# Kernel optimization log

Measured on AMD Instinct MI355X. Metric: run time of the kernel, lower is better.

## Reference

```python
import math
import jax, jax.numpy as jnp
import numpy as np

N = 512
C_S, C_Z, C_H, H, PQ, PV = 384, 128, 16, 12, 4, 8
INF, EPS = 1e5, 1e-8


def _quat_to_rot(q):
    # q: [N,4] unnormalized quaternions -> [N,3,3] rotation matrices
    q = q / jnp.linalg.norm(q, axis=-1, keepdims=True)
    w, x, y, z = q[:, 0], q[:, 1], q[:, 2], q[:, 3]
    return jnp.stack([
        jnp.stack([1 - 2 * (y * y + z * z), 2 * (x * y - w * z), 2 * (x * z + w * y)], -1),
        jnp.stack([2 * (x * y + w * z), 1 - 2 * (x * x + z * z), 2 * (y * z - w * x)], -1),
        jnp.stack([2 * (x * z - w * y), 2 * (y * z + w * x), 1 - 2 * (x * x + y * y)], -1),
    ], -2)


def setup_inputs() -> dict:
    key = jax.random.key(0)
    ks = jax.random.split(key, 16)
    sc = 0.02
    inp = {
        "s": jax.random.normal(ks[0], (N, C_S), jnp.float32),
        "z": jax.random.normal(ks[1], (N, N, C_Z), jnp.float32),
        "rot": _quat_to_rot(jax.random.normal(ks[2], (N, 4), jnp.float32)),
        "trans": jax.random.normal(ks[3], (N, 3), jnp.float32) * 10.0,
        "mask": jnp.ones((N,), jnp.float32),
        "Wq": jax.random.normal(ks[4], (C_S, H * C_H), jnp.float32) * sc,
        "bq": jnp.zeros((H * C_H,), jnp.float32),
        "Wkv": jax.random.normal(ks[5], (C_S, 2 * H * C_H), jnp.float32) * sc,
        "bkv": jnp.zeros((2 * H * C_H,), jnp.float32),
        "Wqp": jax.random.normal(ks[6], (C_S, H * 3 * PQ), jnp.float32) * sc,
        "bqp": jnp.zeros((H * 3 * PQ,), jnp.float32),
        "Wkvp": jax.random.normal(ks[7], (C_S, H * 3 * (PQ + PV)), jnp.float32) * sc,
        "bkvp": jnp.zeros((H * 3 * (PQ + PV),), jnp.float32),
        "Wb": jax.random.normal(ks[8], (C_Z, H), jnp.float32) * sc,
        "bb": jnp.zeros((H,), jnp.float32),
        "head_weights": jnp.full((H,), math.log(math.e - 1.0), jnp.float32),
        "Wout": jax.random.normal(ks[9], (H * (C_Z + C_H + PV * 4), C_S), jnp.float32) * sc,
        "bout": jnp.zeros((C_S,), jnp.float32),
    }
    return inp


def _ipa(s, z, rot, trans, mask, Wq, bq, Wkv, bkv, Wqp, bqp, Wkvp, bkvp, Wb, bb, head_weights, Wout, bout):
    q = (s @ Wq + bq).reshape(N, H, C_H)
    kv = (s @ Wkv + bkv).reshape(N, H, 2 * C_H)
    k, v = kv[..., :C_H], kv[..., C_H:]

    def proj_pts(W, b, P):
        # torch: split last dim into 3 chunks, stack on -1 -> layout [N, 3, H, P] -> [N, H, P, 3]
        pl = (s @ W + b).reshape(N, 3, H, P).transpose(0, 2, 3, 1)
        return jnp.einsum('nij,nhpj->nhpi', rot, pl) + trans[:, None, None, :]

    q_pts = proj_pts(Wqp, bqp, PQ)                    # [N,H,PQ,3]
    kv_pts = proj_pts(Wkvp, bkvp, PQ + PV)            # [N,H,PQ+PV,3]
    k_pts, v_pts = kv_pts[..., :PQ, :], kv_pts[..., PQ:, :]

    b_bias = z @ Wb + bb                              # [N,N,H]
    a = jnp.einsum('ihc,jhc->hij', q, k) * math.sqrt(1.0 / (3 * C_H))
    a = a + math.sqrt(1.0 / 3) * b_bias.transpose(2, 0, 1)

    d2 = jnp.sum((q_pts[:, None] - k_pts[None]) ** 2, axis=-1)   # [i,j,H,PQ]
    hw = jax.nn.softplus(head_weights) * math.sqrt(1.0 / (3 * (PQ * 9.0 / 2)))
    pt_att = -0.5 * jnp.sum(d2 * hw[None, None, :, None], axis=-1)  # [i,j,H]

    sq_mask = INF * (mask[:, None] * mask[None, :] - 1.0)
    a = jax.nn.softmax(a + pt_att.transpose(2, 0, 1) + sq_mask[None], axis=-1)  # [H,i,j]

    o = jnp.einsum('hij,jhc->ihc', a, v).reshape(N, H * C_H)
    o_pt = jnp.einsum('hij,jhpc->ihpc', a, v_pts)                 # [i,H,PV,3]
    o_pt = jnp.einsum('nji,nhpj->nhpi', rot, o_pt - trans[:, None, None, :])  # invert_apply
    o_pt_norm = jnp.sqrt(jnp.sum(o_pt ** 2, axis=-1) + EPS).reshape(N, H * PV)
    o_pt_flat = o_pt.reshape(N, H * PV, 3)
    o_pair = jnp.einsum('hij,ijc->ihc', a, z).reshape(N, H * C_Z)

    cat = jnp.concatenate(
        [o, o_pt_flat[..., 0], o_pt_flat[..., 1], o_pt_flat[..., 2], o_pt_norm, o_pair], axis=-1)
    return cat @ Wout + bout


def reference(s, z, rot, trans, mask, Wq, bq, Wkv, bkv, Wqp, bqp, Wkvp, bkvp, Wb, bb, head_weights, Wout, bout):
    return _ipa(s, z, rot, trans, mask, Wq, bq, Wkv, bkv, Wqp, bqp, Wkvp, bkvp, Wb, bb, head_weights, Wout, bout)
```

## Files before the change

### kernel.cpp

```cpp
#include <hip/hip_runtime.h>
#include <math.h>

#define NN 512
#define CS 384
#define CZ 128
#define CH 16
#define HH 12
#define PQ 4
#define PV 8

typedef float f32x4 __attribute__((ext_vector_type(4)));
typedef __bf16 bf16x8 __attribute__((ext_vector_type(8)));

__global__ void k_repack(const float* __restrict__ Wq,  const float* __restrict__ bq,
                         const float* __restrict__ Wkv, const float* __restrict__ bkv,
                         const float* __restrict__ Wqp, const float* __restrict__ bqp,
                         const float* __restrict__ Wkvp,const float* __restrict__ bkvp,
                         float* __restrict__ Wcat, float* __restrict__ bcat)
{
    const int total = CS * 1152;
    for (int idx = blockIdx.x * blockDim.x + threadIdx.x; idx < total; idx += gridDim.x * blockDim.x) {
        int kk = idx / 1152, n = idx % 1152;
        float vv;
        if (n < 192)      vv = Wq  [kk * 192 + n];
        else if (n < 576) vv = Wkv [kk * 384 + (n - 192)];
        else if (n < 720) vv = Wqp [kk * 144 + (n - 576)];
        else              vv = Wkvp[kk * 432 + (n - 720)];
        Wcat[idx] = vv;
    }
    int n = blockIdx.x * blockDim.x + threadIdx.x;
    if (n < 1152) {
        float vv;
        if (n < 192)      vv = bq  [n];
        else if (n < 576) vv = bkv [n - 192];
        else if (n < 720) vv = bqp [n - 576];
        else              vv = bkvp[n - 720];
        bcat[n] = vv;
    }
}

__global__ void k_proj(const float* __restrict__ s, const float* __restrict__ Wcat,
                       const float* __restrict__ bcat,
                       float* __restrict__ q, float* __restrict__ k_t, float* __restrict__ v,
                       float* __restrict__ qp_raw, float* __restrict__ kvp_raw)
{
    __shared__ float As[64 * 68];
    __shared__ float Bs[64 * 64];

    int tx = threadIdx.x & 15;
    int ty = threadIdx.x >> 4;
    int n0 = blockIdx.x * 64;
    int m0 = blockIdx.y * 64;

    float acc[4][4];
    #pragma unroll
    for (int r = 0; r < 4; ++r)
        #pragma unroll
        for (int cc = 0; cc < 4; ++cc) acc[r][cc] = 0.f;

    for (int kb = 0; kb < CS; kb += 64) {
        #pragma unroll
        for (int e = 0; e < 16; ++e) {
            int idx = e * 256 + threadIdx.x;
            int m = idx >> 6, kk = idx & 63;
            As[m * 68 + kk] = s[(size_t)(m0 + m) * CS + kb + kk];
        }
        #pragma unroll
        for (int e = 0; e < 16; ++e) {
            int idx = e * 256 + threadIdx.x;
            int kk = idx >> 6, n = idx & 63;
            Bs[kk * 64 + n] = Wcat[(size_t)(kb + kk) * 1152 + n0 + n];
        }
        __syncthreads();

        for (int kk = 0; kk < 64; kk += 4) {
            f32x4 a[4], b[4];
            #pragma unroll
            for (int r = 0; r < 4; ++r)
                a[r] = *(const f32x4*)&As[(ty * 4 + r) * 68 + kk];
            #pragma unroll
            for (int kq = 0; kq < 4; ++kq)
                b[kq] = *(const f32x4*)&Bs[(kk + kq) * 64 + tx * 4];
            #pragma unroll
            for (int kq = 0; kq < 4; ++kq)
                #pragma unroll
                for (int r = 0; r < 4; ++r)
                    #pragma unroll
                    for (int cc = 0; cc < 4; ++cc)
                        acc[r][cc] += a[r][kq] * b[kq][cc];
        }
        __syncthreads();
    }

    #pragma unroll
    for (int r = 0; r < 4; ++r) {
        int i = m0 + ty * 4 + r;
        #pragma unroll
        for (int cc = 0; cc < 4; ++cc) {
            int col = n0 + tx * 4 + cc;
            float val = acc[r][cc] + bcat[col];
            if (col < 192) {
                q[i * 192 + col] = val;
            } else if (col < 576) {
                int lc = col - 192;
                int h = lc / 32, w = lc % 32;
                if (w < CH) k_t[(h * CH + w) * NN + i] = val;
                else        v[(i * HH + h) * CH + (w - CH)] = val;
            } else if (col < 720) {
                qp_raw[i * 144 + (col - 576)] = val;
            } else {
                kvp_raw[i * 432 + (col - 720)] = val;
            }
        }
    }
}

__global__ void k_pts_transform(const float* __restrict__ qp_raw, const float* __restrict__ kvp_raw,
                                const float* __restrict__ rot, const float* __restrict__ trans,
                                float* __restrict__ q_pts, float* __restrict__ k_pts_t,
                                float* __restrict__ v_pts)
{
    int idx = blockIdx.x * blockDim.x + threadIdx.x;
    const int total = NN * HH * 16;
    if (idx >= total) return;
    int i = idx / (HH * 16);
    int r = idx % (HH * 16);
    int h = r / 16;
    int p = r % 16;

    float R[9], t3[3];
    for (int a = 0; a < 9; ++a) R[a] = rot[i * 9 + a];
    for (int a = 0; a < 3; ++a) t3[a] = trans[i * 3 + a];

    float x, y, zc;
    if (p < PQ) {
        x  = qp_raw[i * 144 + 0 * 48 + h * PQ + p];
        y  = qp_raw[i * 144 + 1 * 48 + h * PQ + p];
        zc = qp_raw[i * 144 + 2 * 48 + h * PQ + p];
    } else {
        int pp = p - PQ;
        x  = kvp_raw[i * 432 + 0 * 144 + h * 12 + pp];
        y  = kvp_raw[i * 432 + 1 * 144 + h * 12 + pp];
        zc = kvp_raw[i * 432 + 2 * 144 + h * 12 + pp];
    }
    float ox = R[0] * x + R[1] * y + R[2] * zc + t3[0];
    float oy = R[3] * x + R[4] * y + R[5] * zc + t3[1];
    float oz = R[6] * x + R[7] * y + R[8] * zc + t3[2];

    if (p < PQ) {
        int o = ((i * HH + h) * PQ + p) * 3;
        q_pts[o] = ox; q_pts[o + 1] = oy; q_pts[o + 2] = oz;
    } else {
        int pp = p - PQ;
        if (pp < PQ) {
            int rb = (h * PQ + pp) * 3;
            k_pts_t[(size_t)(rb + 0) * NN + i] = ox;
            k_pts_t[(size_t)(rb + 1) * NN + i] = oy;
            k_pts_t[(size_t)(rb + 2) * NN + i] = oz;
        } else {
            int o = ((i * HH + h) * PV + (pp - PQ)) * 3;
            v_pts[o] = ox; v_pts[o + 1] = oy; v_pts[o + 2] = oz;
        }
    }
}

__global__ void k_bias(const float* __restrict__ z, const float* __restrict__ Wb,
                       float* __restrict__ b_bias)
{
    int i = blockIdx.x;
    int lane = threadIdx.x & 63;
    int wave = threadIdx.x >> 6;
    int col  = lane & 15;
    int quad = lane >> 4;

    bf16x8 bfrag[4];
    #pragma unroll
    for (int kc = 0; kc < 4; ++kc) {
        #pragma unroll
        for (int jj = 0; jj < 8; ++jj) {
            int c = kc * 32 + quad * 8 + jj;
            float wv = (col < HH) ? Wb[c * HH + col] : 0.0f;
            bfrag[kc][jj] = (__bf16)wv;
        }
    }

    for (int tt = 0; tt < 8; ++tt) {
        int j0 = (wave + 4 * tt) * 16;
        const float* zrow = z + ((size_t)i * NN + j0 + col) * CZ;
        f32x4 acc = {0.f, 0.f, 0.f, 0.f};
        #pragma unroll
        for (int kc = 0; kc < 4; ++kc) {
            float4 z0 = *(const float4*)(zrow + kc * 32 + quad * 8);
            float4 z1 = *(const float4*)(zrow + kc * 32 + quad * 8 + 4);
            bf16x8 afrag;
            afrag[0] = (__bf16)z0.x; afrag[1] = (__bf16)z0.y;
            afrag[2] = (__bf16)z0.z; afrag[3] = (__bf16)z0.w;
            afrag[4] = (__bf16)z1.x; afrag[5] = (__bf16)z1.y;
            afrag[6] = (__bf16)z1.z; afrag[7] = (__bf16)z1.w;
            acc = __builtin_amdgcn_mfma_f32_16x16x32_bf16(afrag, bfrag[kc], acc, 0, 0, 0);
        }
        if (col < HH) {
            #pragma unroll
            for (int r = 0; r < 4; ++r) {
                int j = j0 + quad * 4 + r;
                b_bias[((size_t)col * NN + i) * NN + j] = acc[r];
            }
        }
    }
}

__global__ void k_logits(const float* __restrict__ b_bias, const float* __restrict__ bb,
                         const float* __restrict__ q, const float* __restrict__ k_t,
                         const float* __restrict__ q_pts, const float* __restrict__ k_pts_t,
                         const float* __restrict__ head_weights,
                         const float* __restrict__ mask,
                         float* __restrict__ a_out)
{
    __shared__ float lgs[HH][NN];
    __shared__ float q_lds[HH * CH];
    __shared__ float qp_lds[HH * PQ * 3];
    __shared__ float hw_lds[HH];

    int i = blockIdx.x;
    int j = threadIdx.x;

    for (int t = j; t < HH * CH; t += 512) q_lds[t] = q[i * HH * CH + t];
    for (int t = j; t < HH * PQ * 3; t += 512) qp_lds[t] = q_pts[i * HH * PQ * 3 + t];
    if (j < HH) {
        float x = head_weights[j];
        hw_lds[j] = log1pf(expf(x)) * sqrtf(1.0f / 54.0f);
    }
    __syncthreads();

    const float qk_scale = sqrtf(1.0f / 48.0f);
    const float b_scale  = sqrtf(1.0f / 3.0f);
    float sqm = 100000.0f * (mask[i] * mask[j] - 1.0f);

    #pragma unroll
    for (int h = 0; h < HH; ++h) {
        float bias_h = b_bias[((size_t)h * NN + i) * NN + j] + bb[h];
        float acc = 0.f;
        #pragma unroll
        for (int c = 0; c < CH; ++c)
            acc += q_lds[h * CH + c] * k_t[(size_t)(h * CH + c) * NN + j];
        float s2 = 0.f;
        #pragma unroll
        for (int p = 0; p < PQ; ++p) {
            int rb = (h * PQ + p) * 3;
            float dx = qp_lds[rb + 0] - k_pts_t[(size_t)(rb + 0) * NN + j];
            float dy = qp_lds[rb + 1] - k_pts_t[(size_t)(rb + 1) * NN + j];
            float dz = qp_lds[rb + 2] - k_pts_t[(size_t)(rb + 2) * NN + j];
            s2 += dx * dx + dy * dy + dz * dz;
        }
        lgs[h][j] = acc * qk_scale + b_scale * bias_h - 0.5f * hw_lds[h] * s2 + sqm;
    }
    __syncthreads();

    int wave = j >> 6, lane = j & 63;
    for (int row = wave; row < HH; row += 8) {
        float vals[8];
        float m = -1e30f;
        #pragma unroll
        for (int u = 0; u < 8; ++u) { vals[u] = lgs[row][lane + u * 64]; m = fmaxf(m, vals[u]); }
        #pragma unroll
        for (int off = 32; off >= 1; off >>= 1) m = fmaxf(m, __shfl_xor(m, off));
        float ssum = 0.f;
        #pragma unroll
        for (int u = 0; u < 8; ++u) { vals[u] = expf(vals[u] - m); ssum += vals[u]; }
        #pragma unroll
        for (int off = 32; off >= 1; off >>= 1) ssum += __shfl_xor(ssum, off);
        float inv = 1.0f / ssum;
        #pragma unroll
        for (int u = 0; u < 8; ++u) lgs[row][lane + u * 64] = vals[u] * inv;
    }
    __syncthreads();

    #pragma unroll
    for (int h = 0; h < HH; ++h)
        a_out[((size_t)h * NN + i) * NN + j] = lgs[h][j];
}

__global__ void k_out_ov(const float* __restrict__ a, const float* __restrict__ v,
                         const float* __restrict__ v_pts,
                         const float* __restrict__ rot, const float* __restrict__ trans,
                         float* __restrict__ cat)
{
    __shared__ float a_lds[HH][NN];
    __shared__ float opt_lds[HH * PV * 3];
    int i = blockIdx.x;
    for (int h = 0; h < HH; ++h)
        for (int j = threadIdx.x; j < NN; j += 256)
            a_lds[h][j] = a[((size_t)h * NN + i) * NN + j];
    __syncthreads();

    for (int out = threadIdx.x; out < 480; out += 256) {
        float acc = 0.f;
        if (out < 192) {
            int h = out / CH;
            for (int j = 0; j < NN; ++j)
                acc += a_lds[h][j] * v[(size_t)j * 192 + out];
            cat[(size_t)i * 2112 + out] = acc;
        } else {
            int r = out - 192;
            int h = r / (PV * 3);
            for (int j = 0; j < NN; ++j)
                acc += a_lds[h][j] * v_pts[(size_t)j * (HH * PV * 3) + r];
            opt_lds[r] = acc;
        }
    }
    __syncthreads();

    if (threadIdx.x < HH * PV) {
        int hp = threadIdx.x;
        float R[9], t3[3];
        for (int a2 = 0; a2 < 9; ++a2) R[a2] = rot[i * 9 + a2];
        for (int a2 = 0; a2 < 3; ++a2) t3[a2] = trans[i * 3 + a2];
        float gx = opt_lds[hp * 3 + 0] - t3[0];
        float gy = opt_lds[hp * 3 + 1] - t3[1];
        float gz = opt_lds[hp * 3 + 2] - t3[2];
        float lx = R[0] * gx + R[3] * gy + R[6] * gz;
        float ly = R[1] * gx + R[4] * gy + R[7] * gz;
        float lz = R[2] * gx + R[5] * gy + R[8] * gz;
        float* crow = cat + (size_t)i * 2112;
        crow[192 + 0 * 96 + hp] = lx;
        crow[192 + 1 * 96 + hp] = ly;
        crow[192 + 2 * 96 + hp] = lz;
        crow[480 + hp] = sqrtf(lx * lx + ly * ly + lz * lz + 1e-8f);
    }
}

#define ALDS_STRIDE 516
__global__ void __launch_bounds__(256)
k_out_pair(const float* __restrict__ a, const float* __restrict__ z,
           float* __restrict__ cat)
{
    __shared__ float a_lds[HH * ALDS_STRIDE];

    int i = blockIdx.x;
    int tid = threadIdx.x;
    int lane = tid & 63;
    int wave = tid >> 6;
    int col  = lane & 15;
    int quad = lane >> 4;

    for (int t = tid; t < HH * NN; t += 256) {
        int h = t >> 9, j = t & 511;
        a_lds[h * ALDS_STRIDE + j] = a[((size_t)h * NN + i) * NN + j];
    }
    __syncthreads();

    int hc = (col < HH) ? col : (HH - 1);
    f32x4 acc0 = {0.f, 0.f, 0.f, 0.f};
    f32x4 acc1 = {0.f, 0.f, 0.f, 0.f};
    int c0 = (wave * 2 + 0) * 16 + col;
    int c1 = (wave * 2 + 1) * 16 + col;

    for (int ks = 0; ks < 16; ++ks) {
        int k0 = ks * 32 + quad * 8;
        const float* arow = &a_lds[hc * ALDS_STRIDE + k0];
        bf16x8 af;
        #pragma unroll
        for (int jj = 0; jj < 8; ++jj) af[jj] = (__bf16)arow[jj];

        const float* zrow = z + ((size_t)i * NN + k0) * CZ;
        bf16x8 bf0, bf1;
        #pragma unroll
        for (int jj = 0; jj < 8; ++jj) bf0[jj] = (__bf16)zrow[(size_t)jj * CZ + c0];
        #pragma unroll
        for (int jj = 0; jj < 8; ++jj) bf1[jj] = (__bf16)zrow[(size_t)jj * CZ + c1];

        acc0 = __builtin_amdgcn_mfma_f32_16x16x32_bf16(af, bf0, acc0, 0, 0, 0);
        acc1 = __builtin_amdgcn_mfma_f32_16x16x32_bf16(af, bf1, acc1, 0, 0, 0);
    }

    float* crow = cat + (size_t)i * 2112 + 576;
    #pragma unroll
    for (int r = 0; r < 4; ++r) {
        int h = quad * 4 + r;
        if (h < HH) {
            crow[h * CZ + c0] = acc0[r];
            crow[h * CZ + c1] = acc1[r];
        }
    }
}

__global__ void k_final(const float* __restrict__ cat, const float* __restrict__ Wout,
                        const float* __restrict__ bout, float* __restrict__ out)
{
    __shared__ float As[64 * 52];
    __shared__ float Bs[48 * 64];

    int tx = threadIdx.x & 15;
    int ty = threadIdx.x >> 4;
    int n0 = blockIdx.x * 64;
    int m0 = blockIdx.y * 64;
    int k0 = blockIdx.z * 528;

    float acc[4][4];
    #pragma unroll
    for (int r = 0; r < 4; ++r)
        #pragma unroll
        for (int cc = 0; cc < 4; ++cc) acc[r][cc] = 0.f;

    for (int stage = 0; stage < 11; ++stage) {
        int kb = k0 + stage * 48;
        #pragma unroll
        for (int e = 0; e < 12; ++e) {
            int idx = e * 256 + threadIdx.x;
            int m = idx / 48, kk = idx % 48;
            As[m * 52 + kk] = cat[(size_t)(m0 + m) * 2112 + kb + kk];
        }
        #pragma unroll
        for (int e = 0; e < 12; ++e) {
            int idx = e * 256 + threadIdx.x;
            int kk = idx >> 6, n = idx & 63;
            Bs[kk * 64 + n] = Wout[(size_t)(kb + kk) * 384 + n0 + n];
        }
        __syncthreads();

        for (int kk = 0; kk < 48; kk += 4) {
            f32x4 a[4], b[4];
            #pragma unroll
            for (int r = 0; r < 4; ++r)
                a[r] = *(const f32x4*)&As[(ty * 4 + r) * 52 + kk];
            #pragma unroll
            for (int kq = 0; kq < 4; ++kq)
                b[kq] = *(const f32x4*)&Bs[(kk + kq) * 64 + tx * 4];
            #pragma unroll
            for (int kq = 0; kq < 4; ++kq)
                #pragma unroll
                for (int r = 0; r < 4; ++r)
                    #pragma unroll
                    for (int cc = 0; cc < 4; ++cc)
                        acc[r][cc] += a[r][kq] * b[kq][cc];
        }
        __syncthreads();
    }

    bool add_bias = (blockIdx.z == 0);
    #pragma unroll
    for (int r = 0; r < 4; ++r) {
        int m = m0 + ty * 4 + r;
        #pragma unroll
        for (int cc = 0; cc < 4; ++cc) {
            int n = n0 + tx * 4 + cc;
            float val = acc[r][cc] + (add_bias ? bout[n] : 0.f);
            atomicAdd(&out[(size_t)m * 384 + n], val);
        }
    }
}

extern "C" void kernel_launch(void* const* d_in, const int* in_sizes, int n_in,
                              void* d_out, int out_size, void* d_ws, size_t ws_size,
                              hipStream_t stream)
{
    const float* s     = (const float*)d_in[0];
    const float* z     = (const float*)d_in[1];
    const float* rot   = (const float*)d_in[2];
    const float* trans = (const float*)d_in[3];
    const float* mask  = (const float*)d_in[4];
    const float* Wq    = (const float*)d_in[5];
    const float* bq    = (const float*)d_in[6];
    const float* Wkv   = (const float*)d_in[7];
    const float* bkv   = (const float*)d_in[8];
    const float* Wqp   = (const float*)d_in[9];
    const float* bqp   = (const float*)d_in[10];
    const float* Wkvp  = (const float*)d_in[11];
    const float* bkvp  = (const float*)d_in[12];
    const float* Wb    = (const float*)d_in[13];
    const float* bb    = (const float*)d_in[14];
    const float* hw    = (const float*)d_in[15];
    const float* Wout  = (const float*)d_in[16];
    const float* bout  = (const float*)d_in[17];
    float* out = (float*)d_out;

    float* ws = (float*)d_ws;
    float* q       = ws;
    float* k_t     = ws + 98304;
    float* v       = ws + 196608;
    float* qp_raw  = ws + 294912;
    float* kvp_raw = ws + 368640;
    float* q_pts   = ws + 589824;
    float* k_pts_t = ws + 663552;
    float* v_pts   = ws + 737280;
    float* a_buf   = ws + 884736;
    float* b_bias  = ws + 4030464;
    float* cat     = ws + 7176192;
    float* Wcat    = ws + 8257536;
    float* bcat    = ws + 8699904;

    hipMemsetAsync(out, 0, (size_t)NN * CS * sizeof(float), stream);

    hipLaunchKernelGGL(k_repack, dim3(512), dim3(256), 0, stream,
                       Wq, bq, Wkv, bkv, Wqp, bqp, Wkvp, bkvp, Wcat, bcat);
    hipLaunchKernelGGL(k_proj, dim3(18, 8), dim3(256), 0, stream,
                       s, Wcat, bcat, q, k_t, v, qp_raw, kvp_raw);
    hipLaunchKernelGGL(k_pts_transform, dim3(384), dim3(256), 0, stream,
                       qp_raw, kvp_raw, rot, trans, q_pts, k_pts_t, v_pts);
    hipLaunchKernelGGL(k_bias, dim3(NN), dim3(256), 0, stream, z, Wb, b_bias);
    hipLaunchKernelGGL(k_logits, dim3(NN), dim3(512), 0, stream,
                       b_bias, bb, q, k_t, q_pts, k_pts_t, hw, mask, a_buf);
    hipLaunchKernelGGL(k_out_ov, dim3(NN), dim3(256), 0, stream,
                       a_buf, v, v_pts, rot, trans, cat);
    hipLaunchKernelGGL(k_out_pair, dim3(NN), dim3(256), 0, stream, a_buf, z, cat);
    hipLaunchKernelGGL(k_final, dim3(6, 8, 4), dim3(256), 0, stream, cat, Wout, bout, out);
}
```

Before: 413.4 us.

## Fuse pair bias, logits, softmax and output aggregation into one attention kernel

Result: slower. 431.9 us (+4.5%).

```diff
diff --git a/kernel.cpp b/kernel.cpp
--- a/kernel.cpp
+++ b/kernel.cpp
@@ -8,9 +8,11 @@
 #define HH 12
 #define PQ 4
 #define PV 8
+#define LGS_S 516
 
 typedef float f32x4 __attribute__((ext_vector_type(4)));
 typedef __bf16 bf16x8 __attribute__((ext_vector_type(8)));
+typedef __bf16 bf16x4 __attribute__((ext_vector_type(4)));
 
 __global__ void k_repack(const float* __restrict__ Wq,  const float* __restrict__ bq,
                          const float* __restrict__ Wkv, const float* __restrict__ bkv,
@@ -164,85 +166,19 @@
     }
 }
 
-__global__ void k_bias(const float* __restrict__ z, const float* __restrict__ Wb,
-                       float* __restrict__ b_bias)
-{
-    int i = blockIdx.x;
-    int lane = threadIdx.x & 63;
-    int wave = threadIdx.x >> 6;
-    int col  = lane & 15;
-    int quad = lane >> 4;
-
-    bf16x8 bfrag[4];
-    #pragma unroll
-    for (int kc = 0; kc < 4; ++kc) {
-        #pragma unroll
-        for (int jj = 0; jj < 8; ++jj) {
-            int c = kc * 32 + quad * 8 + jj;
-            float wv = (col < HH) ? Wb[c * HH + col] : 0.0f;
-            bfrag[kc][jj] = (__bf16)wv;
-        }
-    }
-
-    for (int tt = 0; tt < 8; ++tt) {
-        int j0 = (wave + 4 * tt) * 16;
-        const float* zrow = z + ((size_t)i * NN + j0 + col) * CZ;
-        f32x4 acc = {0.f, 0.f, 0.f, 0.f};
-        #pragma unroll
-        for (int kc = 0; kc < 4; ++kc) {
-            float4 z0 = *(const float4*)(zrow + kc * 32 + quad * 8);
-            float4 z1 = *(const float4*)(zrow + kc * 32 + quad * 8 + 4);
-            bf16x8 afrag;
-            afrag[0] = (__bf16)z0.x; afrag[1] = (__bf16)z0.y;
-            afrag[2] = (__bf16)z0.z; afrag[3] = (__bf16)z0.w;
-            afrag[4] = (__bf16)z1.x; afrag[5] = (__bf16)z1.y;
-            afrag[6] = (__bf16)z1.z; afrag[7] = (__bf16)z1.w;
-            acc = __builtin_amdgcn_mfma_f32_16x16x32_bf16(afrag, bfrag[kc], acc, 0, 0, 0);
-        }
-        if (col < HH) {
-            #pragma unroll
-            for (int r = 0; r < 4; ++r) {
-                int j = j0 + quad * 4 + r;
-                b_bias[((size_t)col * NN + i) * NN + j] = acc[r];
-            }
-        }
-    }
-}
-
-__global__ void k_logits(const float* __restrict__ b_bias, const float* __restrict__ bb,
-                         const float* __restrict__ q, const float* __restrict__ k_t,
-                         const float* __restrict__ q_pts, const float* __restrict__ k_pts_t,
-                         const float* __restrict__ head_weights,
-                         const float* __restrict__ mask,
-                         float* __restrict__ a_out)
-{
-    __shared__ float lgs[HH][NN];
-    __shared__ float q_lds[HH * CH];
-    __shared__ float qp_lds[HH * PQ * 3];
-    __shared__ float hw_lds[HH];
-
-    int i = blockIdx.x;
-    int j = threadIdx.x;
-
-    for (int t = j; t < HH * CH; t += 512) q_lds[t] = q[i * HH * CH + t];
-    for (int t = j; t < HH * PQ * 3; t += 512) qp_lds[t] = q_pts[i * HH * PQ * 3 + t];
-    if (j < HH) {
-        float x = head_weights[j];
-        hw_lds[j] = log1pf(expf(x)) * sqrtf(1.0f / 54.0f);
-    }
-    __syncthreads();
-
-    const float qk_scale = sqrtf(1.0f / 48.0f);
-    const float b_scale  = sqrtf(1.0f / 3.0f);
-    float sqm = 100000.0f * (mask[i] * mask[j] - 1.0f);
-
-    #pragma unroll
-    for (int h = 0; h < HH; ++h) {
-        float bias_h = b_bias[((size_t)h * NN + i) * NN + j] + bb[h];
-        float acc = 0.f;
+__device__ __forceinline__ void ipa_logits_rows(
+    int hbeg, int hend, int j,
+    const float* __restrict__ k_t, const float* __restrict__ k_pts_t,
+    const float* q_lds, const float* qp_lds, const float* hw_lds, const float* bb_l,
+    float sqm, float (*lgs)[LGS_S])
+{
+    const float qk_scale = 0.14433756729740643f;
+    const float b_scale  = 0.57735026918962576f;
+    for (int h = hbeg; h < hend; ++h) {
+        float accq = 0.f;
         #pragma unroll
         for (int c = 0; c < CH; ++c)
-            acc += q_lds[h * CH + c] * k_t[(size_t)(h * CH + c) * NN + j];
+            accq += q_lds[h * CH + c] * k_t[(size_t)(h * CH + c) * NN + j];
         float s2 = 0.f;
         #pragma unroll
         for (int p = 0; p < PQ; ++p) {
@@ -252,11 +188,117 @@
             float dz = qp_lds[rb + 2] - k_pts_t[(size_t)(rb + 2) * NN + j];
             s2 += dx * dx + dy * dy + dz * dz;
         }
-        lgs[h][j] = acc * qk_scale + b_scale * bias_h - 0.5f * hw_lds[h] * s2 + sqm;
+        lgs[h][j] = accq * qk_scale + b_scale * bb_l[h] - 0.5f * hw_lds[h] * s2 + sqm;
+    }
+}
+
+__global__ void __launch_bounds__(512, 2)
+k_attn(const float* __restrict__ z, const float* __restrict__ Wb,
+       const float* __restrict__ bb,
+       const float* __restrict__ q, const float* __restrict__ k_t,
+       const float* __restrict__ q_pts, const float* __restrict__ k_pts_t,
+       const float* __restrict__ head_weights, const float* __restrict__ mask,
+       const float* __restrict__ v, const float* __restrict__ v_pts,
+       const float* __restrict__ rot, const float* __restrict__ trans,
+       float* __restrict__ cat)
+{
+    __shared__ __bf16 zl[NN * CZ];
+    __shared__ float lgs[HH][LGS_S];
+    __shared__ float q_lds[HH * CH];
+    __shared__ float qp_lds[HH * PQ * 3];
+    __shared__ float hw_lds[HH];
+    __shared__ float bb_l[HH];
+    __shared__ float opt_lds[HH * PV * 3];
+
+    const int i = blockIdx.x;
+    const int tid = threadIdx.x;
+    const int lane = tid & 63;
+    const int wave = tid >> 6;
+    const float* zbase = z + (size_t)i * NN * CZ;
+
+    f32x4 zr[16];
+    #pragma unroll
+    for (int e = 0; e < 16; ++e)
+        zr[e] = *(const f32x4*)(zbase + ((e * 512 + tid) << 2));
+
+    if (tid < HH * CH)     q_lds[tid]  = q[(size_t)i * HH * CH + tid];
+    if (tid < HH * PQ * 3) qp_lds[tid] = q_pts[(size_t)i * HH * PQ * 3 + tid];
+    if (tid < HH) {
+        float x = head_weights[tid];
+        hw_lds[tid] = log1pf(expf(x)) * 0.13608276348795434f;
+        bb_l[tid] = bb[tid];
+    }
+    asm volatile("s_waitcnt lgkmcnt(0)" ::: "memory");
+    __builtin_amdgcn_s_barrier();
+
+    const float sqm = 100000.0f * (mask[i] * mask[tid] - 1.0f);
+
+    ipa_logits_rows(0, 6, tid, k_t, k_pts_t, q_lds, qp_lds, hw_lds, bb_l, sqm, lgs);
+
+    #pragma unroll
+    for (int e = 0; e < 16; ++e) {
+        int f = e * 512 + tid;
+        int j = f >> 5;
+        int c0 = (f & 31) << 2;
+        bf16x4 w;
+        w[0] = (__bf16)zr[e][0]; w[1] = (__bf16)zr[e][1];
+        w[2] = (__bf16)zr[e][2]; w[3] = (__bf16)zr[e][3];
+        *(bf16x4*)&zl[j * CZ + (c0 ^ ((j & 7) << 3))] = w;
+    }
+    #pragma unroll
+    for (int e = 0; e < 16; ++e)
+        zr[e] = *(const f32x4*)(zbase + (((e + 16) * 512 + tid) << 2));
+
+    ipa_logits_rows(6, 12, tid, k_t, k_pts_t, q_lds, qp_lds, hw_lds, bb_l, sqm, lgs);
+
+    #pragma unroll
+    for (int e = 0; e < 16; ++e) {
+        int f = (e + 16) * 512 + tid;
+        int j = f >> 5;
+        int c0 = (f & 31) << 2;
+        bf16x4 w;
+        w[0] = (__bf16)zr[e][0]; w[1] = (__bf16)zr[e][1];
+        w[2] = (__bf16)zr[e][2]; w[3] = (__bf16)zr[e][3];
+        *(bf16x4*)&zl[j * CZ + (c0 ^ ((j & 7) << 3))] = w;
     }
     __syncthreads();
 
-    int wave = j >> 6, lane = j & 63;
+    {
+        const float b_scale = 0.57735026918962576f;
+        const int hcol = lane & 15;
+        const int q8 = (lane >> 4) * 8;
+        bf16x8 wbf[4];
+        #pragma unroll
+        for (int kc = 0; kc < 4; ++kc) {
+            #pragma unroll
+            for (int jj = 0; jj < 8; ++jj) {
+                int c = kc * 32 + q8 + jj;
+                float wv = (hcol < HH) ? Wb[c * HH + hcol] * b_scale : 0.0f;
+                wbf[kc][jj] = (__bf16)wv;
+            }
+        }
+        #pragma unroll
+        for (int t = 0; t < 4; ++t) {
+            int j0 = (wave * 4 + t) * 16;
+            int jrow = j0 + (lane & 15);
+            int swz = (jrow & 7) << 3;
+            f32x4 acc = {0.f, 0.f, 0.f, 0.f};
+            #pragma unroll
+            for (int kc = 0; kc < 4; ++kc) {
+                bf16x8 af = *(const bf16x8*)&zl[jrow * CZ + ((kc * 32 + q8) ^ swz)];
+                acc = __builtin_amdgcn_mfma_f32_16x16x32_bf16(af, wbf[kc], acc, 0, 0, 0);
+            }
+            if (hcol < HH) {
+                #pragma unroll
+                for (int r = 0; r < 4; ++r) {
+                    int j = j0 + (lane >> 4) * 4 + r;
+                    lgs[hcol][j] += acc[r];
+                }
+            }
+        }
+    }
+    __syncthreads();
+
     for (int row = wave; row < HH; row += 8) {
         float vals[8];
         float m = -1e30f;
@@ -275,45 +317,62 @@
     }
     __syncthreads();
 
-    #pragma unroll
-    for (int h = 0; h < HH; ++h)
-        a_out[((size_t)h * NN + i) * NN + j] = lgs[h][j];
-}
-
-__global__ void k_out_ov(const float* __restrict__ a, const float* __restrict__ v,
-                         const float* __restrict__ v_pts,
-                         const float* __restrict__ rot, const float* __restrict__ trans,
-                         float* __restrict__ cat)
-{
-    __shared__ float a_lds[HH][NN];
-    __shared__ float opt_lds[HH * PV * 3];
-    int i = blockIdx.x;
-    for (int h = 0; h < HH; ++h)
-        for (int j = threadIdx.x; j < NN; j += 256)
-            a_lds[h][j] = a[((size_t)h * NN + i) * NN + j];
+    if (tid < 480) {
+        float acc = 0.f;
+        if (tid < 192) {
+            const float* lr = lgs[tid >> 4];
+            const float* vp = v + tid;
+            #pragma unroll 4
+            for (int j = 0; j < NN; ++j)
+                acc += lr[j] * vp[(size_t)j * 192];
+            cat[(size_t)i * 2112 + tid] = acc;
+        } else {
+            int r = tid - 192;
+            const float* lr = lgs[r / 24];
+            const float* vp = v_pts + r;
+            #pragma unroll 4
+            for (int j = 0; j < NN; ++j)
+                acc += lr[j] * vp[(size_t)j * 288];
+            opt_lds[r] = acc;
+        }
+    }
+
+    {
+        int cl = lane & 15;
+        int q4 = lane >> 4;
+        int ha = (cl < HH) ? cl : (HH - 1);
+        int cb = wave * 16 + cl;
+        f32x4 pacc = {0.f, 0.f, 0.f, 0.f};
+        for (int ks = 0; ks < 16; ++ks) {
+            int jb = ks * 32 + q4 * 8;
+            f32x4 a0 = *(const f32x4*)&lgs[ha][jb];
+            f32x4 a1 = *(const f32x4*)&lgs[ha][jb + 4];
+            bf16x8 af;
+            af[0] = (__bf16)a0[0]; af[1] = (__bf16)a0[1];
+            af[2] = (__bf16)a0[2]; af[3] = (__bf16)a0[3];
+            af[4] = (__bf16)a1[0]; af[5] = (__bf16)a1[1];
+            af[6] = (__bf16)a1[2]; af[7] = (__bf16)a1[3];
+            bf16x8 bf;
+            #pragma unroll
+            for (int jj = 0; jj < 8; ++jj)
+                bf[jj] = zl[(jb + jj) * CZ + (cb ^ (jj << 3))];
+            pacc = __builtin_amdgcn_mfma_f32_16x16x32_bf16(af, bf, pacc, 0, 0, 0);
+        }
+        float* crow = cat + (size_t)i * 2112 + 576;
+        #pragma unroll
+        for (int r = 0; r < 4; ++r) {
+            int h = q4 * 4 + r;
+            if (h < HH) crow[h * CZ + cb] = pacc[r];
+        }
+    }
     __syncthreads();
 
-    for (int out = threadIdx.x; out < 480; out += 256) {
-        float acc = 0.f;
-        if (out < 192) {
-            int h = out / CH;
-            for (int j = 0; j < NN; ++j)
-                acc += a_lds[h][j] * v[(size_t)j * 192 + out];
-            cat[(size_t)i * 2112 + out] = acc;
-        } else {
-            int r = out - 192;
-            int h = r / (PV * 3);
-            for (int j = 0; j < NN; ++j)
-                acc += a_lds[h][j] * v_pts[(size_t)j * (HH * PV * 3) + r];
-            opt_lds[r] = acc;
-        }
-    }
-    __syncthreads();
-
-    if (threadIdx.x < HH * PV) {
-        int hp = threadIdx.x;
+    if (tid < HH * PV) {
+        int hp = tid;
         float R[9], t3[3];
+        #pragma unroll
         for (int a2 = 0; a2 < 9; ++a2) R[a2] = rot[i * 9 + a2];
+        #pragma unroll
         for (int a2 = 0; a2 < 3; ++a2) t3[a2] = trans[i * 3 + a2];
         float gx = opt_lds[hp * 3 + 0] - t3[0];
         float gy = opt_lds[hp * 3 + 1] - t3[1];
@@ -326,61 +385,6 @@
         crow[192 + 1 * 96 + hp] = ly;
         crow[192 + 2 * 96 + hp] = lz;
         crow[480 + hp] = sqrtf(lx * lx + ly * ly + lz * lz + 1e-8f);
-    }
-}
-
-#define ALDS_STRIDE 516
-__global__ void __launch_bounds__(256)
-k_out_pair(const float* __restrict__ a, const float* __restrict__ z,
-           float* __restrict__ cat)
-{
-    __shared__ float a_lds[HH * ALDS_STRIDE];
-
-    int i = blockIdx.x;
-    int tid = threadIdx.x;
-    int lane = tid & 63;
-    int wave = tid >> 6;
-    int col  = lane & 15;
-    int quad = lane >> 4;
-
-    for (int t = tid; t < HH * NN; t += 256) {
-        int h = t >> 9, j = t & 511;
-        a_lds[h * ALDS_STRIDE + j] = a[((size_t)h * NN + i) * NN + j];
-    }
-    __syncthreads();
-
-    int hc = (col < HH) ? col : (HH - 1);
-    f32x4 acc0 = {0.f, 0.f, 0.f, 0.f};
-    f32x4 acc1 = {0.f, 0.f, 0.f, 0.f};
-    int c0 = (wave * 2 + 0) * 16 + col;
-    int c1 = (wave * 2 + 1) * 16 + col;
-
-    for (int ks = 0; ks < 16; ++ks) {
-        int k0 = ks * 32 + quad * 8;
-        const float* arow = &a_lds[hc * ALDS_STRIDE + k0];
-        bf16x8 af;
-        #pragma unroll
-        for (int jj = 0; jj < 8; ++jj) af[jj] = (__bf16)arow[jj];
-
-        const float* zrow = z + ((size_t)i * NN + k0) * CZ;
-        bf16x8 bf0, bf1;
-        #pragma unroll
-        for (int jj = 0; jj < 8; ++jj) bf0[jj] = (__bf16)zrow[(size_t)jj * CZ + c0];
-        #pragma unroll
-        for (int jj = 0; jj < 8; ++jj) bf1[jj] = (__bf16)zrow[(size_t)jj * CZ + c1];
-
-        acc0 = __builtin_amdgcn_mfma_f32_16x16x32_bf16(af, bf0, acc0, 0, 0, 0);
-        acc1 = __builtin_amdgcn_mfma_f32_16x16x32_bf16(af, bf1, acc1, 0, 0, 0);
-    }
-
-    float* crow = cat + (size_t)i * 2112 + 576;
-    #pragma unroll
-    for (int r = 0; r < 4; ++r) {
-        int h = quad * 4 + r;
-        if (h < HH) {
-            crow[h * CZ + c0] = acc0[r];
-            crow[h * CZ + c1] = acc1[r];
-        }
     }
 }
 
@@ -483,11 +487,9 @@
     float* q_pts   = ws + 589824;
     float* k_pts_t = ws + 663552;
     float* v_pts   = ws + 737280;
-    float* a_buf   = ws + 884736;
-    float* b_bias  = ws + 4030464;
-    float* cat     = ws + 7176192;
-    float* Wcat    = ws + 8257536;
-    float* bcat    = ws + 8699904;
+    float* cat     = ws + 884736;
+    float* Wcat    = ws + 1966080;
+    float* bcat    = ws + 2408448;
 
     hipMemsetAsync(out, 0, (size_t)NN * CS * sizeof(float), stream);
 
@@ -497,11 +499,8 @@
                        s, Wcat, bcat, q, k_t, v, qp_raw, kvp_raw);
     hipLaunchKernelGGL(k_pts_transform, dim3(384), dim3(256), 0, stream,
                        qp_raw, kvp_raw, rot, trans, q_pts, k_pts_t, v_pts);
-    hipLaunchKernelGGL(k_bias, dim3(NN), dim3(256), 0, stream, z, Wb, b_bias);
-    hipLaunchKernelGGL(k_logits, dim3(NN), dim3(512), 0, stream,
-                       b_bias, bb, q, k_t, q_pts, k_pts_t, hw, mask, a_buf);
-    hipLaunchKernelGGL(k_out_ov, dim3(NN), dim3(256), 0, stream,
-                       a_buf, v, v_pts, rot, trans, cat);
-    hipLaunchKernelGGL(k_out_pair, dim3(NN), dim3(256), 0, stream, a_buf, z, cat);
+    hipLaunchKernelGGL(k_attn, dim3(NN), dim3(512), 0, stream,
+                       z, Wb, bb, q, k_t, q_pts, k_pts_t, hw, mask,
+                       v, v_pts, rot, trans, cat);
     hipLaunchKernelGGL(k_final, dim3(6, 8, 4), dim3(256), 0, stream, cat, Wout, bout, out);
 }
```
